# Kernel optimization log

Hardware: AMD Instinct MI355X
Metric: run time of the kernel (lower is better)

The kernel has to match this reference:

```python
import jax, jax.numpy as jnp
import numpy as np

B, S, D, H = 4, 1024, 512, 8
NEG = -1e9


def setup_inputs() -> dict:
    key = jax.random.key(0)
    ks = jax.random.split(key, 16)
    s = 0.02
    inp = {
        "query": jax.random.normal(ks[0], (B, S, D), dtype=jnp.float32),
        "key": jax.random.normal(ks[1], (B, S, D), dtype=jnp.float32),
        "value": jax.random.normal(ks[2], (B, S, D), dtype=jnp.float32),
        "mask": jax.random.randint(ks[3], (B, 1, S), 0, 2, dtype=jnp.int32),
        "mask_p": jax.random.randint(ks[4], (B, 1, S), 0, 2, dtype=jnp.int32),
        # multi-head projections: d_model -> d_model*h
        "Wq": jax.random.normal(ks[5], (D, H * D), dtype=jnp.float32) * s,
        "bq": jnp.zeros((H * D,), dtype=jnp.float32),
        "Wk": jax.random.normal(ks[6], (D, H * D), dtype=jnp.float32) * s,
        "bk": jnp.zeros((H * D,), dtype=jnp.float32),
        "Wv": jax.random.normal(ks[7], (D, H * D), dtype=jnp.float32) * s,
        "bv": jnp.zeros((H * D,), dtype=jnp.float32),
        # single-head p-branch projections: d_model -> d_model
        "Wpq": jax.random.normal(ks[8], (D, D), dtype=jnp.float32) * s,
        "bpq": jnp.zeros((D,), dtype=jnp.float32),
        "Wpk": jax.random.normal(ks[9], (D, D), dtype=jnp.float32) * s,
        "bpk": jnp.zeros((D,), dtype=jnp.float32),
        "Wpv": jax.random.normal(ks[10], (D, D), dtype=jnp.float32) * s,
        "bpv": jnp.zeros((D,), dtype=jnp.float32),
        # output projection
        "Wo": jax.random.normal(ks[11], (D, D), dtype=jnp.float32) * s,
        "bo": jnp.zeros((D,), dtype=jnp.float32),
    }
    return inp


def _attn(q, k, v, mask4):
    # q,k,v: [B,h,S,d]; mask4: [B,1,1,S] or None. Dropout omitted (eval mode).
    d = q.shape[-1]
    scores = jnp.einsum('bhqd,bhkd->bhqk', q, k) / jnp.sqrt(jnp.asarray(d, q.dtype))
    if mask4 is not None:
        scores = jnp.where(mask4 == 0, jnp.asarray(NEG, scores.dtype), scores)
    p = jax.nn.softmax(scores, axis=-1)
    return jnp.einsum('bhqk,bhkd->bhqd', p, v)


def reference(query, key, value, mask, mask_p,
              Wq, bq, Wk, bk, Wv, bv,
              Wpq, bpq, Wpk, bpk, Wpv, bpv, Wo, bo):
    nb, sl, d = query.shape
    def proj(x, W, b, heads):
        return (x @ W + b).reshape(nb, sl, heads, d).transpose(0, 2, 1, 3)

    m4 = mask[:, None, :, :]    # [B,1,1,S]
    mp4 = mask_p[:, None, :, :]

    qx = proj(query, Wq, bq, H)
    kx = proj(key, Wk, bk, H)
    vx = proj(value, Wv, bv, H)
    x = _attn(qx, kx, vx, m4)            # [B,H,S,D]

    qp = proj(query, Wpq, bpq, 1)
    kp = proj(key, Wpk, bpk, 1)
    vp = proj(value, Wpv, bpv, 1)
    x_p = _attn(qp, kp, vp, mp4)         # [B,1,S,D]

    # squared distance per head, softmax over heads at each (b, s)
    dis = jnp.sum((x - x_p) ** 2, axis=3)          # [B,H,S]
    w = jax.nn.softmax(1.0 / (dis + 1e-9), axis=1)  # [B,H,S]
    output = jnp.einsum('bhs,bhsd->bsd', w, x)      # [B,S,D]

    mixed = output * 0.8 + x_p[:, 0] * 0.2
    return mixed @ Wo + bo
```

## Files before the change

### kernel.cpp

```cpp
#include <hip/hip_runtime.h>
#include <cstdint>

#define S_LEN   1024
#define D_DIM   512
#define H_HEADS 8
#define B_BATCH 4
#define NEGV    -1000000000.0f

typedef __bf16 bf16;
typedef __bf16 bf16x8 __attribute__((ext_vector_type(8)));
typedef __bf16 bf16x4 __attribute__((ext_vector_type(4)));
typedef float  f32x4  __attribute__((ext_vector_type(4)));

#define GLL16(gp, lp) __builtin_amdgcn_global_load_lds( \
    (const __attribute__((address_space(1))) void*)(gp), \
    (__attribute__((address_space(3))) void*)(lp), 16, 0, 0)

#define VMW(N) asm volatile("s_waitcnt vmcnt(" #N ")" ::: "memory")
#define BARM() do { asm volatile("" ::: "memory"); \
                    __builtin_amdgcn_s_barrier();  \
                    asm volatile("" ::: "memory"); } while (0)

template<int MODE>
__global__ __launch_bounds__(512, 2) void gemm256_bt(
    const bf16* __restrict__ A, const bf16* __restrict__ B,
    void* __restrict__ Cout, const float* __restrict__ bias,
    const float* __restrict__ bias2, const int* __restrict__ mask,
    const int* __restrict__ maskp,
    int N, int K, long zsA, long zsB, long zsC, float scale)
{
  const int gx = gridDim.x, gy = gridDim.y;
  const int nwg = gx * gy * gridDim.z;
  int bid = blockIdx.x + gx * (blockIdx.y + gy * blockIdx.z);
  {
    const int q = nwg >> 3, r = nwg & 7;
    const int xcd = bid & 7, idx = bid >> 3;
    bid = (xcd < r ? xcd * (q + 1) : r * (q + 1) + (xcd - r) * q) + idx;
  }
  const int bx = bid % gx;
  const int by = (bid / gx) % gy;
  const int z  = bid / (gx * gy);

  A += (long)z * zsA;
  B += (long)z * zsB;
  const int bm0 = bx * 256;
  const int bn0 = by * 256;

  __shared__ __attribute__((aligned(16))) bf16 LDS[4 * 16384];

  const int tid  = threadIdx.x;
  const int wid  = tid >> 6;
  const int lane = tid & 63;
  const int wr = wid >> 2;
  const int wc = wid & 3;

  const long arow = (long)(bm0 + wid * 16 + (lane & 15)) * K + ((lane >> 4) * 8);
  const long brow = (long)(bn0 + wid * 16 + (lane & 15)) * K + ((lane >> 4) * 8);
  const long rstep = 128L * (long)K;

  auto stageA = [&](int tt) {
    bf16* d = LDS + (tt & 3) * 16384 + wid * 512;
    const bf16* g = A + arow + (long)tt * 32;
    GLL16(g, d);
    GLL16(g + rstep, d + 4096);
  };
  auto stageB = [&](int tt) {
    bf16* d = LDS + (tt & 3) * 16384 + 8192 + wid * 512;
    const bf16* g = B + brow + (long)tt * 32;
    GLL16(g, d);
    GLL16(g + rstep, d + 4096);
  };

  f32x4 acc[8][4] = {};
  const int NT = K >> 5;

  stageA(0); stageB(0);
  stageA(1); stageB(1);
  stageA(2); stageB(2);
  VMW(8);
  BARM();

  for (int t = 0; t < NT; ++t) {
    const bf16* bufp = LDS + (t & 3) * 16384;
    const bf16* ap = bufp + wr * 4096 + lane * 8;
    const bf16* bp = bufp + 8192 + wc * 2048 + lane * 8;

    if (t + 3 < NT) { stageA(t + 3); stageB(t + 3); }

    bf16x8 a0[4], a1[4], bb[4];
#pragma unroll
    for (int i = 0; i < 4; ++i) a0[i] = *(const bf16x8*)(ap + i * 512);
#pragma unroll
    for (int i = 0; i < 4; ++i) bb[i] = *(const bf16x8*)(bp + i * 512);
#pragma unroll
    for (int i = 0; i < 4; ++i) a1[i] = *(const bf16x8*)(ap + (4 + i) * 512);

    __builtin_amdgcn_s_setprio(1);
#pragma unroll
    for (int mi = 0; mi < 4; ++mi)
#pragma unroll
      for (int ni = 0; ni < 4; ++ni)
        acc[mi][ni] = __builtin_amdgcn_mfma_f32_16x16x32_bf16(
            a0[mi], bb[ni], acc[mi][ni], 0, 0, 0);
#pragma unroll
    for (int mi = 0; mi < 4; ++mi)
#pragma unroll
      for (int ni = 0; ni < 4; ++ni)
        acc[4 + mi][ni] = __builtin_amdgcn_mfma_f32_16x16x32_bf16(
            a1[mi], bb[ni], acc[4 + mi][ni], 0, 0, 0);
    __builtin_amdgcn_s_setprio(0);

    if (t <= NT - 4)      VMW(8);
    else if (t == NT - 3) VMW(4);
    else if (t == NT - 2) VMW(0);
    BARM();
  }

  const int r0 = (lane >> 4) << 2;
  const int cn = lane & 15;

#pragma unroll
  for (int mi = 0; mi < 8; ++mi) {
#pragma unroll
    for (int ni = 0; ni < 4; ++ni) {
      const int n = bn0 + wc * 64 + ni * 16 + cn;
      float bv = 0.f;
      if constexpr (MODE != 4) {
        const float* bp2 = (z == 1 && bias2) ? bias2 : bias;
        if (bp2) bv = bp2[n];
      }
      int mk = 1;
      if constexpr (MODE == 4) {
        const int* mp = (z >= 32 ? maskp : mask);
        mk = mp[(z & 3) * S_LEN + n];
      }
#pragma unroll
      for (int r = 0; r < 4; ++r) {
        const int m = bm0 + wr * 128 + mi * 16 + r0 + r;
        float v = acc[mi][ni][r];
        if constexpr (MODE == 1) {
          long o = (long)z * zsC +
                   (((long)(n >> 9) * B_BATCH + (m >> 10)) * S_LEN + (m & (S_LEN - 1))) * D_DIM
                   + (n & (D_DIM - 1));
          ((bf16*)Cout)[o] = (bf16)(v + bv);
        } else if constexpr (MODE == 2) {
          long o = (long)z * zsC +
                   (((long)(n >> 9) * B_BATCH + (m >> 10)) * D_DIM + (n & (D_DIM - 1))) * S_LEN
                   + (m & (S_LEN - 1));
          ((bf16*)Cout)[o] = (bf16)(v + bv);
        } else if constexpr (MODE == 3) {
          ((float*)Cout)[(long)z * zsC + (long)m * N + n] = v + bv;
        } else {
          float sv = (mk == 0) ? NEGV : v * scale;
          ((bf16*)Cout)[(long)z * zsC + (long)m * N + n] = (bf16)sv;
        }
      }
    }
  }
}

template<int MODE>
__global__ __launch_bounds__(256) void gemm_bt(
    const bf16* __restrict__ A, const bf16* __restrict__ B,
    void* __restrict__ Cout, const float* __restrict__ bias,
    const float* __restrict__ bias2, const int* __restrict__ mask,
    int N, int K, long zsA, long zsB, long zsC, float scale, int Hh)
{
  const int z = blockIdx.z;
  A += (long)z * zsA;
  B += (long)z * zsB;

  const int bm0 = blockIdx.x * 128;
  const int bn0 = blockIdx.y * 128;

  __shared__ __attribute__((aligned(16))) bf16 As[128 * 32];
  __shared__ __attribute__((aligned(16))) bf16 Bs[128 * 32];

  const int tid  = threadIdx.x;
  const int wid  = tid >> 6;
  const int lane = tid & 63;
  const int wm = (wid >> 1) * 64;
  const int wn = (wid & 1) * 64;

  const int srow = tid >> 2;
  const int scol = (tid & 3) * 8;
  const bf16* gA0 = A + (long)(bm0 + srow) * K + scol;
  const bf16* gA1 = A + (long)(bm0 + 64 + srow) * K + scol;
  const bf16* gB0 = B + (long)(bn0 + srow) * K + scol;
  const bf16* gB1 = B + (long)(bn0 + 64 + srow) * K + scol;
  bf16* lA0 = As + tid * 8;
  bf16* lA1 = As + 2048 + tid * 8;
  bf16* lB0 = Bs + tid * 8;
  bf16* lB1 = Bs + 2048 + tid * 8;

  const int lrow = lane & 15;
  const int lk   = (lane >> 4) * 8;
  const bf16* fA = As + (wm + lrow) * 32 + lk;
  const bf16* fB = Bs + (wn + lrow) * 32 + lk;

  f32x4 acc[4][4] = {};

  for (int k0 = 0; k0 < K; k0 += 32) {
    GLL16(gA0 + k0, lA0);
    GLL16(gA1 + k0, lA1);
    GLL16(gB0 + k0, lB0);
    GLL16(gB1 + k0, lB1);
    __syncthreads();
    bf16x8 af[4], bfr[4];
#pragma unroll
    for (int i = 0; i < 4; ++i) af[i]  = *(const bf16x8*)(fA + i * 16 * 32);
#pragma unroll
    for (int i = 0; i < 4; ++i) bfr[i] = *(const bf16x8*)(fB + i * 16 * 32);
#pragma unroll
    for (int mi = 0; mi < 4; ++mi)
#pragma unroll
      for (int ni = 0; ni < 4; ++ni)
        acc[mi][ni] = __builtin_amdgcn_mfma_f32_16x16x32_bf16(
            af[mi], bfr[ni], acc[mi][ni], 0, 0, 0);
    __syncthreads();
  }

  const int r0 = (lane >> 4) << 2;
  const int cn = lane & 15;

#pragma unroll
  for (int mi = 0; mi < 4; ++mi) {
#pragma unroll
    for (int ni = 0; ni < 4; ++ni) {
      const int n = bn0 + wn + ni * 16 + cn;
      float bv = 0.f;
      const float* bp = (z == 1 && bias2) ? bias2 : bias;
      if (bp) bv = bp[n];
#pragma unroll
      for (int r = 0; r < 4; ++r) {
        const int m = bm0 + wm + mi * 16 + r0 + r;
        float v = acc[mi][ni][r];
        if constexpr (MODE == 3) {
          ((float*)Cout)[(long)z * zsC + (long)m * N + n] = v + bv;
        }
      }
    }
  }
  (void)mask; (void)scale; (void)Hh;
}

__global__ __launch_bounds__(256) void softmax_rows(bf16* __restrict__ buf)
{
  const long row = blockIdx.x;
  bf16* p = buf + row * S_LEN;
  const int tid = threadIdx.x;
  const int wid = tid >> 6, lane = tid & 63;
  bf16x4 raw = *(const bf16x4*)(p + tid * 4);
  float v[4];
#pragma unroll
  for (int j = 0; j < 4; ++j) v[j] = (float)raw[j];
  float mx = fmaxf(fmaxf(v[0], v[1]), fmaxf(v[2], v[3]));
  for (int m = 32; m; m >>= 1) mx = fmaxf(mx, __shfl_xor(mx, m, 64));
  __shared__ float red[4];
  if (lane == 0) red[wid] = mx;
  __syncthreads();
  mx = fmaxf(fmaxf(red[0], red[1]), fmaxf(red[2], red[3]));
  float e[4]; float s = 0.f;
#pragma unroll
  for (int j = 0; j < 4; ++j) { e[j] = __expf(v[j] - mx); s += e[j]; }
  for (int m = 32; m; m >>= 1) s += __shfl_xor(s, m, 64);
  __syncthreads();
  if (lane == 0) red[wid] = s;
  __syncthreads();
  s = red[0] + red[1] + red[2] + red[3];
  const float inv = 1.f / s;
  bf16x4 o;
#pragma unroll
  for (int j = 0; j < 4; ++j) o[j] = (bf16)(e[j] * inv);
  *(bf16x4*)(p + tid * 4) = o;
}

__global__ __launch_bounds__(256) void combine_kernel(
    const float* __restrict__ X, const float* __restrict__ XP,
    bf16* __restrict__ MIX)
{
  const int m = blockIdx.x;
  const int b = m >> 10;
  const int s = m & (S_LEN - 1);
  const int tid = threadIdx.x;
  const int wid = tid >> 6, lane = tid & 63;
  const float2 xp = *(const float2*)(XP + (long)m * D_DIM + tid * 2);
  float xv0[H_HEADS], xv1[H_HEADS], part[H_HEADS];
#pragma unroll
  for (int h = 0; h < H_HEADS; ++h) {
    const float* xrow = X + ((long)(h * B_BATCH + b) * S_LEN + s) * D_DIM;
    float2 t = *(const float2*)(xrow + tid * 2);
    xv0[h] = t.x; xv1[h] = t.y;
    float d0 = t.x - xp.x, d1 = t.y - xp.y;
    part[h] = d0 * d0 + d1 * d1;
  }
  __shared__ float red[4][H_HEADS];
#pragma unroll
  for (int h = 0; h < H_HEADS; ++h) {
    float v = part[h];
    for (int mm = 32; mm; mm >>= 1) v += __shfl_xor(v, mm, 64);
    if (lane == 0) red[wid][h] = v;
  }
  __syncthreads();
  float w[H_HEADS]; float mx = -1e30f;
#pragma unroll
  for (int h = 0; h < H_HEADS; ++h) {
    float dis = red[0][h] + red[1][h] + red[2][h] + red[3][h];
    w[h] = 1.f / (dis + 1e-9f);
    mx = fmaxf(mx, w[h]);
  }
  float ssum = 0.f;
#pragma unroll
  for (int h = 0; h < H_HEADS; ++h) { w[h] = __expf(w[h] - mx); ssum += w[h]; }
  const float inv = 1.f / ssum;
  float m0 = 0.f, m1 = 0.f;
#pragma unroll
  for (int h = 0; h < H_HEADS; ++h) { m0 += w[h] * xv0[h]; m1 += w[h] * xv1[h]; }
  m0 = 0.8f * m0 * inv + 0.2f * xp.x;
  m1 = 0.8f * m1 * inv + 0.2f * xp.y;
  const bf16 h0 = (bf16)m0, h1 = (bf16)m1;
  const bf16 l0 = (bf16)(m0 - (float)h0), l1 = (bf16)(m1 - (float)h1);
  bf16* orow = MIX + (long)m * 1536;
  orow[tid * 2]        = h0; orow[tid * 2 + 1]        = h1;
  orow[512 + tid * 2]  = l0; orow[512 + tid * 2 + 1]  = l1;
  orow[1024 + tid * 2] = h0; orow[1024 + tid * 2 + 1] = h1;
}

__global__ __launch_bounds__(256) void cvt3_kernel(
    const float* __restrict__ s0, const float* __restrict__ s1, const float* __restrict__ s2,
    bf16* __restrict__ d0, bf16* __restrict__ d1, bf16* __restrict__ d2)
{
  const float* s = blockIdx.z == 0 ? s0 : (blockIdx.z == 1 ? s1 : s2);
  bf16* d       = blockIdx.z == 0 ? d0 : (blockIdx.z == 1 ? d1 : d2);
  const long i = ((long)blockIdx.x * 256 + threadIdx.x) * 8;
  float4 a = *(const float4*)(s + i);
  float4 b = *(const float4*)(s + i + 4);
  bf16x8 o;
  o[0]=(bf16)a.x; o[1]=(bf16)a.y; o[2]=(bf16)a.z; o[3]=(bf16)a.w;
  o[4]=(bf16)b.x; o[5]=(bf16)b.y; o[6]=(bf16)b.z; o[7]=(bf16)b.w;
  *(bf16x8*)(d + i) = o;
}

__global__ __launch_bounds__(256) void concat_bias(
    const float* __restrict__ b0, const float* __restrict__ p0,
    const float* __restrict__ b1, const float* __restrict__ p1,
    const float* __restrict__ b2, const float* __restrict__ p2,
    float* __restrict__ o0, float* __restrict__ o1, float* __restrict__ o2)
{
  const int i = blockIdx.x * 256 + threadIdx.x;
  const float* bb; const float* pp; float* oo;
  if (blockIdx.y == 0)      { bb = b0; pp = p0; oo = o0; }
  else if (blockIdx.y == 1) { bb = b1; pp = p1; oo = o1; }
  else                      { bb = b2; pp = p2; oo = o2; }
  oo[i] = (i < 4096) ? bb[i] : pp[i - 4096];
}

template<int TRIPLE>
__global__ __launch_bounds__(256) void transpose_cvt3(
    const float* __restrict__ s0, const float* __restrict__ s1, const float* __restrict__ s2,
    bf16* __restrict__ d0, bf16* __restrict__ d1, bf16* __restrict__ d2,
    int R, int C)
{
  const float* src = blockIdx.z == 0 ? s0 : (blockIdx.z == 1 ? s1 : s2);
  bf16* dst       = blockIdx.z == 0 ? d0 : (blockIdx.z == 1 ? d1 : d2);
  __shared__ float t[32][33];
  const int tc = threadIdx.x & 31;
  const int tr = threadIdx.x >> 5;
  const int c0 = blockIdx.x * 32, r0 = blockIdx.y * 32;
#pragma unroll
  for (int i = 0; i < 4; ++i)
    t[tr + 8 * i][tc] = src[(long)(r0 + tr + 8 * i) * C + c0 + tc];
  __syncthreads();
  const int RD = TRIPLE ? 3 * R : R;
#pragma unroll
  for (int i = 0; i < 4; ++i) {
    float v = t[tc][tr + 8 * i];
    long o = (long)(c0 + tr + 8 * i) * RD + r0 + tc;
    const bf16 hi = (bf16)v;
    dst[o] = hi;
    if (TRIPLE) {
      dst[o + R] = hi;
      dst[o + 2 * R] = (bf16)(v - (float)hi);
    }
  }
}

extern "C" void kernel_launch(void* const* d_in, const int* in_sizes, int n_in,
                              void* d_out, int out_size, void* d_ws, size_t ws_size,
                              hipStream_t stream) {
  const float* query  = (const float*)d_in[0];
  const float* key    = (const float*)d_in[1];
  const float* value  = (const float*)d_in[2];
  const int*   mask   = (const int*)d_in[3];
  const int*   mask_p = (const int*)d_in[4];
  const float* Wq  = (const float*)d_in[5];  const float* bq  = (const float*)d_in[6];
  const float* Wk  = (const float*)d_in[7];  const float* bk  = (const float*)d_in[8];
  const float* Wv  = (const float*)d_in[9];  const float* bv  = (const float*)d_in[10];
  const float* Wpq = (const float*)d_in[11]; const float* bpq = (const float*)d_in[12];
  const float* Wpk = (const float*)d_in[13]; const float* bpk = (const float*)d_in[14];
  const float* Wpv = (const float*)d_in[15]; const float* bpv = (const float*)d_in[16];
  const float* Wo  = (const float*)d_in[17]; const float* bo  = (const float*)d_in[18];

  char* ws = (char*)d_ws;
  size_t off = 0;
  auto alloc = [&](size_t bytes) -> void* {
    void* p = ws + off;
    off += (bytes + 255) & ~(size_t)255;
    return p;
  };
  const long BS   = (long)B_BATCH * S_LEN;
  const long ZSD  = (long)S_LEN * D_DIM;
  const long ZSS  = (long)S_LEN * S_LEN;
  const long SD   = BS * D_DIM;
  const long DD   = (long)D_DIM * D_DIM;
  const long WSTR = SD + DD;
  const long HSD  = 9L * B_BATCH * ZSD;

  bf16* WQT  = (bf16*)alloc(SD * 2);
  bf16* WPQT = (bf16*)alloc(DD * 2);
  bf16* WKT  = (bf16*)alloc(SD * 2);
  bf16* WPKT = (bf16*)alloc(DD * 2);
  bf16* WVT  = (bf16*)alloc(SD * 2);
  bf16* WPVT = (bf16*)alloc(DD * 2);
  bf16* WOT3 = (bf16*)alloc(3 * DD * 2);
  float* BQ9 = (float*)alloc(4608 * 4);
  float* BK9 = (float*)alloc(4608 * 4);
  float* BV9 = (float*)alloc(4608 * 4);
  bf16* XQ16 = (bf16*)alloc(SD * 2);
  bf16* XK16 = (bf16*)alloc(SD * 2);
  bf16* XV16 = (bf16*)alloc(SD * 2);
  bf16* MIX  = XQ16;
  bf16* Q16  = (bf16*)alloc(HSD * 2);
  bf16* K16  = (bf16*)alloc(HSD * 2);
  float* X   = (float*)Q16;
  float* XP  = X + 32 * ZSD;
  bf16* VT9  = (bf16*)alloc(HSD * 2);
  bf16* SC   = (bf16*)alloc(36L * ZSS * 2);
  (void)in_sizes; (void)n_in; (void)out_size;

  if (off > ws_size) return;

  const dim3 blk(256);
  const dim3 blk512(512);
  const float scale = 0.044194173824159216f;

  cvt3_kernel<<<dim3(1024, 1, 3), blk, 0, stream>>>(query, key, value, XQ16, XK16, XV16);
  concat_bias<<<dim3(18, 3), blk, 0, stream>>>(bq, bpq, bk, bpk, bv, bpv, BQ9, BK9, BV9);
  transpose_cvt3<0><<<dim3(128, 16, 3), blk, 0, stream>>>(Wq, Wk, Wv, WQT, WKT, WVT, 512, 4096);
  transpose_cvt3<0><<<dim3(16, 16, 3), blk, 0, stream>>>(Wpq, Wpk, Wpv, WPQT, WPKT, WPVT, 512, 512);
  transpose_cvt3<1><<<dim3(16, 16, 1), blk, 0, stream>>>(Wo, Wo, Wo, WOT3, WOT3, WOT3, 512, 512);

  gemm256_bt<1><<<dim3(16, 18, 2), blk512, 0, stream>>>(XQ16, WQT, Q16, BQ9, BK9,
      nullptr, nullptr, 4608, 512, SD, WSTR, HSD, 1.f);
  gemm256_bt<2><<<dim3(16, 18, 1), blk512, 0, stream>>>(XV16, WVT, VT9, BV9, nullptr,
      nullptr, nullptr, 4608, 512, 0, 0, 0, 1.f);

  gemm256_bt<4><<<dim3(4, 4, 36), blk512, 0, stream>>>(Q16, K16, SC, nullptr, nullptr,
      mask, mask_p, 1024, 512, ZSD, ZSD, ZSS, scale);

  softmax_rows<<<dim3(36864), blk, 0, stream>>>(SC);

  gemm256_bt<3><<<dim3(4, 2, 36), blk512, 0, stream>>>(SC, VT9, X, nullptr, nullptr,
      nullptr, nullptr, 512, 1024, ZSS, ZSD, ZSD, 1.f);

  combine_kernel<<<dim3(4096), blk, 0, stream>>>(X, XP, MIX);

  gemm_bt<3><<<dim3(32, 4, 1), blk, 0, stream>>>(MIX, WOT3, d_out, bo, nullptr, nullptr,
      512, 1536, 0, 0, 0, 1.f, 1);
}
```

Baseline: 495.5 us.

## Restructure GEMM mainloop into double-buffered 64-wide K tiles with phased staging

The bf16 GEMM mainloop changes from a 4-deep ring of 32-wide K tiles to two buffers of 64-wide K tiles. Each tile is split into four MFMA phases, with the next tile's A/B loads interleaved between phases and barriers around each phase, in the style of an 8-wave ping-pong schedule. The goal is to overlap global-to-LDS transfers with MFMA work while cutting per-iteration waits and register pressure (one A fragment set live instead of two). It adds many more barriers per iteration and less prefetch depth, which may expose memory latency.

Result: no change. 492.2 us (-0.7%).

```diff
diff --git a/kernel.cpp b/kernel.cpp
--- a/kernel.cpp
+++ b/kernel.cpp
@@ -46,7 +46,7 @@
   const int bm0 = bx * 256;
   const int bn0 = by * 256;
 
-  __shared__ __attribute__((aligned(16))) bf16 LDS[4 * 16384];
+  __shared__ __attribute__((aligned(16))) bf16 LDS[2 * 32768];
 
   const int tid  = threadIdx.x;
   const int wid  = tid >> 6;
@@ -54,65 +54,104 @@
   const int wr = wid >> 2;
   const int wc = wid & 3;
 
-  const long arow = (long)(bm0 + wid * 16 + (lane & 15)) * K + ((lane >> 4) * 8);
-  const long brow = (long)(bn0 + wid * 16 + (lane & 15)) * K + ((lane >> 4) * 8);
-  const long rstep = 128L * (long)K;
-
-  auto stageA = [&](int tt) {
-    bf16* d = LDS + (tt & 3) * 16384 + wid * 512;
-    const bf16* g = A + arow + (long)tt * 32;
-    GLL16(g, d);
-    GLL16(g + rstep, d + 4096);
+  const int frow = lane & 15;
+  const int fcol = (lane >> 4) * 8;
+  const bf16* gA0 = A + (long)(bm0 + (2 * wid) * 16 + frow) * K + fcol;
+  const bf16* gA1 = A + (long)(bm0 + (2 * wid + 1) * 16 + frow) * K + fcol;
+  const bf16* gB0 = B + (long)(bn0 + (2 * wid) * 16 + frow) * K + fcol;
+  const bf16* gB1 = B + (long)(bn0 + (2 * wid + 1) * 16 + frow) * K + fcol;
+
+  auto stgA = [&](int t, int kk) {
+    bf16* d = LDS + ((t & 1) << 15) + (kk << 13) + (2 * wid) * 512;
+    const long c = (long)t * 64 + kk * 32;
+    GLL16(gA0 + c, d);
+    GLL16(gA1 + c, d + 512);
   };
-  auto stageB = [&](int tt) {
-    bf16* d = LDS + (tt & 3) * 16384 + 8192 + wid * 512;
-    const bf16* g = B + brow + (long)tt * 32;
-    GLL16(g, d);
-    GLL16(g + rstep, d + 4096);
+  auto stgB = [&](int t, int kk) {
+    bf16* d = LDS + ((t & 1) << 15) + 16384 + (kk << 13) + (2 * wid) * 512;
+    const long c = (long)t * 64 + kk * 32;
+    GLL16(gB0 + c, d);
+    GLL16(gB1 + c, d + 512);
   };
+  auto rdA = [&](int buf, int kk, int mi) -> const bf16* {
+    return LDS + (buf << 15) + (kk << 13) + (wr * 8 + mi) * 512 + lane * 8;
+  };
+  auto rdB = [&](int buf, int kk, int ni) -> const bf16* {
+    return LDS + (buf << 15) + 16384 + (kk << 13) + (wc * 4 + ni) * 512 + lane * 8;
+  };
 
   f32x4 acc[8][4] = {};
-  const int NT = K >> 5;
-
-  stageA(0); stageB(0);
-  stageA(1); stageB(1);
-  stageA(2); stageB(2);
-  VMW(8);
+  const int NT = K >> 6;
+
+  stgA(0, 0); stgB(0, 0); stgA(0, 1); stgB(0, 1);
+  VMW(4);
   BARM();
 
   for (int t = 0; t < NT; ++t) {
-    const bf16* bufp = LDS + (t & 3) * 16384;
-    const bf16* ap = bufp + wr * 4096 + lane * 8;
-    const bf16* bp = bufp + 8192 + wc * 2048 + lane * 8;
-
-    if (t + 3 < NT) { stageA(t + 3); stageB(t + 3); }
-
-    bf16x8 a0[4], a1[4], bb[4];
-#pragma unroll
-    for (int i = 0; i < 4; ++i) a0[i] = *(const bf16x8*)(ap + i * 512);
-#pragma unroll
-    for (int i = 0; i < 4; ++i) bb[i] = *(const bf16x8*)(bp + i * 512);
-#pragma unroll
-    for (int i = 0; i < 4; ++i) a1[i] = *(const bf16x8*)(ap + (4 + i) * 512);
-
+    const int buf = t & 1;
+    const bool pf = (t + 1 < NT);
+    bf16x8 af[4], bb[4];
+
+    if (pf) stgA(t + 1, 0);
+#pragma unroll
+    for (int i = 0; i < 4; ++i) af[i] = *(const bf16x8*)rdA(buf, 0, i);
+#pragma unroll
+    for (int i = 0; i < 4; ++i) bb[i] = *(const bf16x8*)rdB(buf, 0, i);
+    BARM();
     __builtin_amdgcn_s_setprio(1);
 #pragma unroll
     for (int mi = 0; mi < 4; ++mi)
 #pragma unroll
       for (int ni = 0; ni < 4; ++ni)
         acc[mi][ni] = __builtin_amdgcn_mfma_f32_16x16x32_bf16(
-            a0[mi], bb[ni], acc[mi][ni], 0, 0, 0);
+            af[mi], bb[ni], acc[mi][ni], 0, 0, 0);
+    __builtin_amdgcn_s_setprio(0);
+    BARM();
+
+    if (pf) stgB(t + 1, 0);
+#pragma unroll
+    for (int i = 0; i < 4; ++i) af[i] = *(const bf16x8*)rdA(buf, 0, 4 + i);
+    if (pf) { VMW(4); } else { VMW(0); }
+    BARM();
+    __builtin_amdgcn_s_setprio(1);
 #pragma unroll
     for (int mi = 0; mi < 4; ++mi)
 #pragma unroll
       for (int ni = 0; ni < 4; ++ni)
         acc[4 + mi][ni] = __builtin_amdgcn_mfma_f32_16x16x32_bf16(
-            a1[mi], bb[ni], acc[4 + mi][ni], 0, 0, 0);
+            af[mi], bb[ni], acc[4 + mi][ni], 0, 0, 0);
     __builtin_amdgcn_s_setprio(0);
-
-    if (t <= NT - 4)      VMW(8);
-    else if (t == NT - 3) VMW(4);
-    else if (t == NT - 2) VMW(0);
+    BARM();
+
+    if (pf) stgA(t + 1, 1);
+#pragma unroll
+    for (int i = 0; i < 4; ++i) af[i] = *(const bf16x8*)rdA(buf, 1, i);
+#pragma unroll
+    for (int i = 0; i < 4; ++i) bb[i] = *(const bf16x8*)rdB(buf, 1, i);
+    BARM();
+    __builtin_amdgcn_s_setprio(1);
+#pragma unroll
+    for (int mi = 0; mi < 4; ++mi)
+#pragma unroll
+      for (int ni = 0; ni < 4; ++ni)
+        acc[mi][ni] = __builtin_amdgcn_mfma_f32_16x16x32_bf16(
+            af[mi], bb[ni], acc[mi][ni], 0, 0, 0);
+    __builtin_amdgcn_s_setprio(0);
+    BARM();
+
+    if (pf) stgB(t + 1, 1);
+#pragma unroll
+    for (int i = 0; i < 4; ++i) af[i] = *(const bf16x8*)rdA(buf, 1, 4 + i);
+    if (pf) VMW(4);
+    BARM();
+    __builtin_amdgcn_s_setprio(1);
+#pragma unroll
+    for (int mi = 0; mi < 4; ++mi)
+#pragma unroll
+      for (int ni = 0; ni < 4; ++ni)
+        acc[4 + mi][ni] = __builtin_amdgcn_mfma_f32_16x16x32_bf16(
+            af[mi], bb[ni], acc[4 + mi][ni], 0, 0, 0);
+    __builtin_amdgcn_s_setprio(0);
     BARM();
   }
 
```
